# Kernel optimization log

Measured on AMD Instinct MI355X. Metric: run time of the kernel, lower is better.

The kernel has to match this reference:

```python
import jax, jax.numpy as jnp
import numpy as np
from jax import lax

B, T, C = 8, 1025, 512
HEADS = 8
CACHE = 256          # int(dim * cache_ratio)
CLS = 1
L = 256              # gr_cache memory length
H = W = 32           # sqrt(T - CLS)
EPS = 1e-5


def setup_inputs() -> dict:
    key = jax.random.key(0)
    ks = jax.random.split(key, 40)
    def w(k, shape, scale=0.02):
        return jax.random.normal(k, shape, dtype=jnp.float32) * scale
    inp = {}
    inp['x'] = jax.random.normal(ks[0], (B, T, C), dtype=jnp.float32)
    inp['gr_cache'] = jax.random.normal(ks[1], (1, L, CACHE), dtype=jnp.float32)
    # self-attention (dim=512) params, weights stored (in, out)
    inp['Wq1'] = w(ks[2], (C, C)); inp['bq1'] = jnp.zeros((C,), jnp.float32)
    inp['Wk1'] = w(ks[3], (C, C)); inp['bk1'] = jnp.zeros((C,), jnp.float32)
    inp['Wv1'] = w(ks[4], (C, C)); inp['bv1'] = jnp.zeros((C,), jnp.float32)
    inp['Wo1'] = w(ks[5], (C, C)); inp['bo1'] = jnp.zeros((C,), jnp.float32)
    # memory attention (dim=cache_dim=256) params
    inp['Wq2'] = w(ks[6], (CACHE, CACHE)); inp['bq2'] = jnp.zeros((CACHE,), jnp.float32)
    inp['Wk2'] = w(ks[7], (CACHE, CACHE)); inp['bk2'] = jnp.zeros((CACHE,), jnp.float32)
    inp['Wv2'] = w(ks[8], (CACHE, CACHE)); inp['bv2'] = jnp.zeros((CACHE,), jnp.float32)
    inp['Wo2'] = w(ks[9], (CACHE, CACHE)); inp['bo2'] = jnp.zeros((CACHE,), jnp.float32)
    # GRU-style gate linears: in = 2*cache_dim, out = cache_dim
    inp['Wr'] = w(ks[10], (2 * CACHE, CACHE)); inp['br'] = jnp.zeros((CACHE,), jnp.float32)
    inp['Wz'] = w(ks[11], (2 * CACHE, CACHE)); inp['bz'] = jnp.zeros((CACHE,), jnp.float32)
    inp['Wa'] = w(ks[12], (2 * CACHE, CACHE)); inp['ba'] = jnp.zeros((CACHE,), jnp.float32)
    # LayerNorm(cache_dim)
    inp['gamma'] = jnp.ones((CACHE,), jnp.float32)
    inp['beta'] = jnp.zeros((CACHE,), jnp.float32)
    # per-head gate logits, init to -1 as in the module
    inp['lam'] = jnp.full((HEADS,), -1.0, dtype=jnp.float32)
    # grouped conv pos-emb: Conv2d(512, 512, k=3, groups=CACHE) -> (O=512, I/g=2, 3, 3)
    inp['conv_w'] = w(ks[13], (C, C // CACHE, 3, 3))
    inp['conv_b'] = jnp.zeros((C,), jnp.float32)
    return inp


def _mha(q_in, kv_in, Wq, bq, Wk, bk, Wv, bv, Wo, bo):
    Bq, Tq, D = q_in.shape
    Tk = kv_in.shape[1]
    dh = D // HEADS
    q = (q_in @ Wq + bq).reshape(Bq, Tq, HEADS, dh)
    k = (kv_in @ Wk + bk).reshape(Bq, Tk, HEADS, dh)
    v = (kv_in @ Wv + bv).reshape(Bq, Tk, HEADS, dh)
    s = jnp.einsum('bqhd,bkhd->bhqk', q, k) * (1.0 / np.sqrt(dh)).astype(np.float32)
    a = jax.nn.softmax(s, axis=-1)
    o = jnp.einsum('bhqk,bkhd->bqhd', a, v).reshape(Bq, Tq, D)
    return o @ Wo + bo


def reference(x, gr_cache, Wq1, bq1, Wk1, bk1, Wv1, bv1, Wo1, bo1,
              Wq2, bq2, Wk2, bk2, Wv2, bv2, Wo2, bo2,
              Wr, br, Wz, bz, Wa, ba, gamma, beta, lam, conv_w, conv_b):
    B_, T_, C_ = x.shape
    # ---- spatial positional embedding (faithful to torch view->permute quirk) ----
    tok = x[:, CLS:, :].reshape(B_, H, W, C_).transpose(0, 3, 1, 2)   # (B, C, H, W)
    pos = lax.conv_general_dilated(tok, conv_w, (1, 1), 'SAME',
                                   feature_group_count=CACHE,
                                   dimension_numbers=('NCHW', 'OIHW', 'NCHW'))
    pos = pos + conv_b[None, :, None, None]
    pos = pos.reshape(B_, C_, T_ - CLS).transpose(0, 2, 1)            # (B, T-1, C)
    pos = jnp.concatenate([jnp.zeros((B_, CLS, C_), pos.dtype), pos], axis=1)
    # ---- self attention ----
    x_self = _mha(x, x, Wq1, bq1, Wk1, bk1, Wv1, bv1, Wo1, bo1)       # (B, T, C)
    x_self_h = x_self.reshape(B_, T_, HEADS, C_ // HEADS)
    # ---- GRU-style gated cache update ----
    gr = jnp.broadcast_to(gr_cache, (B_, L, CACHE))
    x_summary = x_self[:, :, :CACHE]
    idx = (jnp.arange(L) * T_) // L                                   # nearest interpolate T -> L
    x_summary = x_summary[:, idx, :]                                  # (B, L, CACHE)
    cat = jnp.concatenate([gr, x_summary], axis=-1)
    reset = jax.nn.sigmoid(cat @ Wr + br)
    z = jax.nn.sigmoid(cat @ Wz + bz)
    cat2 = jnp.concatenate([reset * gr, x_summary], axis=-1)
    add = jax.nn.gelu(cat2 @ Wa + ba, approximate=False)
    mu = add.mean(-1, keepdims=True)
    var = ((add - mu) ** 2).mean(-1, keepdims=True)
    add = (add - mu) / jnp.sqrt(var + EPS) * gamma + beta             # LayerNorm
    gr_new = z * add + (1.0 - z) * gr
    # ---- memory attention on first cache_dim channels ----
    x_mem = _mha(x[:, :, :CACHE], gr_new, Wq2, bq2, Wk2, bk2, Wv2, bv2, Wo2, bo2)
    x_mem = x_mem.reshape(B_, T_, HEADS, CACHE // HEADS)
    # ---- per-head alpha blend with zero-padded mem branch ----
    alpha = jax.nn.sigmoid(lam).reshape(1, 1, HEADS, 1)
    pad = jnp.zeros((B_, T_, HEADS, (C_ - CACHE) // HEADS), x.dtype)
    out = (alpha * jnp.concatenate([x_mem, pad], axis=-1)
           + (1.0 - alpha) * x_self_h).reshape(B_, T_, C_) + pos
    return out
```

## Files before the change

kernel.cpp:

```cpp
#include <hip/hip_runtime.h>
#include <math.h>

typedef unsigned short u16;
typedef unsigned int u32;
typedef __attribute__((ext_vector_type(8))) short short8;
typedef __attribute__((ext_vector_type(4))) short short4v;
typedef __attribute__((ext_vector_type(4))) float f32x4;

constexpr int Bc = 8;
constexpr int Tt = 1025;
constexpr int Cc = 512;
constexpr int Hn = 8;
constexpr int CA = 256;
constexpr int Ll = 256;

#if __has_builtin(__builtin_amdgcn_exp2f)
#define EXP2F __builtin_amdgcn_exp2f
#else
#define EXP2F exp2f
#endif

__device__ __forceinline__ u16 f2bf(float f) {
  u32 u = __builtin_bit_cast(u32, f);
  u = (u + 0x7FFFu + ((u >> 16) & 1u)) >> 16;
  return (u16)u;
}
__device__ __forceinline__ u32 pack2f(float lo, float hi) {
  const u32 a = __builtin_bit_cast(u32, hi) + 0x8000u;
  const u32 b = __builtin_bit_cast(u32, lo) + 0x8000u;
  return __builtin_amdgcn_perm(a, b, 0x07060302u);
}

struct WC { const float* s; u16* d; int sN; int sK; int kshift; int tot; };
struct WCP { WC w[11]; };

__global__ void wcast_k(WCP p) {
  const WC a = p.w[blockIdx.y];
  const int kmask = (1 << a.kshift) - 1;
  for (int idx = blockIdx.x * 256 + threadIdx.x; idx < a.tot; idx += gridDim.x * 256) {
    const int k = idx & kmask;
    const int n = idx >> a.kshift;
    a.d[idx] = (k < a.sK) ? f2bf(a.s[(size_t)k * a.sN + n]) : (u16)0;
  }
}

enum { EP_NONE = 0, EP_SIGMOID = 1, EP_GELU = 2 };

struct GemmEpi {
  const float* bias[4];
  int start[4];
  float scale[4];
  int nreg;
};

template <int AF32, int OUTBF, int ACT>
__global__ __launch_bounds__(256) void gemm_mfma(
    const void* __restrict__ Av, int lda,
    const u16* __restrict__ Wt,
    GemmEpi epi,
    void* __restrict__ Cout,
    int M, int N, int K)
{
  __shared__ u16 As[128][32];
  __shared__ u16 Bs[128][32];
  const int tid = threadIdx.x;
  const int m0 = blockIdx.y * 128, n0 = blockIdx.x * 128;
  const int ln = tid & 15, quad = (tid >> 4) & 3, wv = tid >> 6;
  const int wm = (wv & 1) * 64, wn = (wv >> 1) * 64;
  const int sr = tid >> 1;
  const int sk = (tid & 1) * 16;

  f32x4 zf = {0.f, 0.f, 0.f, 0.f};
  f32x4 acc[4][4];
  #pragma unroll
  for (int i = 0; i < 4; i++)
    #pragma unroll
    for (int j = 0; j < 4; j++) acc[i][j] = zf;

  const short8 z8 = {0, 0, 0, 0, 0, 0, 0, 0};

  for (int k0 = 0; k0 < K; k0 += 32) {
    const int gm = m0 + sr;
    short8 a0 = z8, a1 = z8;
    if (gm < M) {
      if (AF32) {
        const float* p = (const float*)Av + (size_t)gm * lda + k0 + sk;
        const float4 f0 = *(const float4*)(p + 0);
        const float4 f1 = *(const float4*)(p + 4);
        const float4 f2 = *(const float4*)(p + 8);
        const float4 f3 = *(const float4*)(p + 12);
        ((u32*)&a0)[0] = pack2f(f0.x, f0.y);
        ((u32*)&a0)[1] = pack2f(f0.z, f0.w);
        ((u32*)&a0)[2] = pack2f(f1.x, f1.y);
        ((u32*)&a0)[3] = pack2f(f1.z, f1.w);
        ((u32*)&a1)[0] = pack2f(f2.x, f2.y);
        ((u32*)&a1)[1] = pack2f(f2.z, f2.w);
        ((u32*)&a1)[2] = pack2f(f3.x, f3.y);
        ((u32*)&a1)[3] = pack2f(f3.z, f3.w);
      } else {
        const u16* p = (const u16*)Av + (size_t)gm * lda + k0 + sk;
        a0 = *(const short8*)p;
        a1 = *(const short8*)(p + 8);
      }
    }
    *(short8*)&As[sr][sk] = a0;
    *(short8*)&As[sr][sk + 8] = a1;
    {
      const u16* q = Wt + (size_t)(n0 + sr) * K + k0 + sk;
      *(short8*)&Bs[sr][sk] = *(const short8*)q;
      *(short8*)&Bs[sr][sk + 8] = *(const short8*)(q + 8);
    }
    __syncthreads();

    short8 af[4], bf[4];
    #pragma unroll
    for (int i = 0; i < 4; i++) af[i] = *(const short8*)&As[wm + i * 16 + ln][quad * 8];
    #pragma unroll
    for (int j = 0; j < 4; j++) bf[j] = *(const short8*)&Bs[wn + j * 16 + ln][quad * 8];
    #pragma unroll
    for (int i = 0; i < 4; i++)
      #pragma unroll
      for (int j = 0; j < 4; j++)
        acc[i][j] = __builtin_amdgcn_mfma_f32_16x16x32_bf16(af[i], bf[j], acc[i][j], 0, 0, 0);
    __syncthreads();
  }

  int ri = 0;
  #pragma unroll
  for (int i = 1; i < 4; i++)
    if (i < epi.nreg && epi.start[i] <= n0) ri = i;
  const float* bp = epi.bias[ri] - epi.start[ri];
  const float sc = epi.scale[ri];

  float bj[4];
  #pragma unroll
  for (int j = 0; j < 4; j++) bj[j] = bp[n0 + wn + j * 16 + ln];

  #pragma unroll
  for (int i = 0; i < 4; i++) {
    #pragma unroll
    for (int r = 0; r < 4; r++) {
      const int gm = m0 + wm + i * 16 + quad * 4 + r;
      if (gm >= M) continue;
      #pragma unroll
      for (int j = 0; j < 4; j++) {
        float v = (acc[i][j][r] + bj[j]) * sc;
        if (ACT == EP_SIGMOID)   v = 1.f / (1.f + __expf(-v));
        else if (ACT == EP_GELU) v = 0.5f * v * (1.f + erff(v * 0.70710678118654752f));
        const size_t off = (size_t)gm * N + n0 + wn + j * 16 + ln;
        if (OUTBF) ((u16*)Cout)[off] = f2bf(v);
        else       ((float*)Cout)[off] = v;
      }
    }
  }
}

template <int DH>
__global__ __launch_bounds__(128) void attn_mfma(
    const u16* __restrict__ Qp, const u16* __restrict__ Kp,
    const u16* __restrict__ Vp, u16* __restrict__ Op,
    int Tq, int Tk, int qbs, int kbs, int obs, int qrs, int krs, int ors)
{
  constexpr int NC = DH / 32;
  constexpr int NM = DH / 16;

  __shared__ u16 Vt[2][DH * 32];
  __shared__ u16 Pb[2 * 32 * 32];

  const int b = blockIdx.y >> 3, h = blockIdx.y & 7;
  const int q0 = blockIdx.x * 64;
  const int tid = threadIdx.x;
  const int wv = tid >> 6;
  const int lane = tid & 63;
  const int ln = lane & 15, quad = lane >> 4;

  const u16* Qb = Qp + (size_t)b * qbs + h * DH;
  const u16* Kb = Kp + (size_t)b * kbs + h * DH;
  const u16* Vb = Vp + (size_t)b * kbs + h * DH;
  u16* Ob = Op + (size_t)b * obs + h * DH;

  const short8 z8 = {0, 0, 0, 0, 0, 0, 0, 0};
  const f32x4 zf = {0.f, 0.f, 0.f, 0.f};

  short8 qf[2][NC];
  #pragma unroll
  for (int qs = 0; qs < 2; qs++) {
    const int gq = q0 + wv * 32 + qs * 16 + ln;
    #pragma unroll
    for (int c = 0; c < NC; c++) {
      if (gq < Tq) qf[qs][c] = *(const short8*)(Qb + (size_t)gq * qrs + c * 32 + quad * 8);
      else         qf[qs][c] = z8;
    }
  }

  f32x4 oacc[2][NM];
  float lsum[2] = {0.f, 0.f};
  #pragma unroll
  for (int qs = 0; qs < 2; qs++)
    #pragma unroll
    for (int c = 0; c < NM; c++) oacc[qs][c] = zf;

  const int vd0 = (tid & 15) * (DH / 16);
  const int vk = (tid >> 4) * 4;
  const int gb = vk >> 3, off = vk & 7;

  const int nfull = Tk >> 5;
  const int nit = (Tk + 31) >> 5;

  for (int it = 0; it < nit; it++) {
    const int k0 = it << 5;
    const bool full = (it < nfull);
    u16* vt = &Vt[it & 1][0];

    short8 kf[2][NC];
    if (full) {
      #pragma unroll
      for (int kc = 0; kc < 2; kc++)
        #pragma unroll
        for (int c = 0; c < NC; c++)
          kf[kc][c] = *(const short8*)(Kb + (size_t)(k0 + kc * 16 + ln) * krs
                                          + c * 32 + quad * 8);
    } else {
      #pragma unroll
      for (int kc = 0; kc < 2; kc++)
        #pragma unroll
        for (int c = 0; c < NC; c++) {
          const int row = k0 + kc * 16 + ln;
          kf[kc][c] = (row < Tk)
              ? *(const short8*)(Kb + (size_t)row * krs + c * 32 + quad * 8)
              : z8;
        }
    }

    {
      short4v vrow[4];
      #pragma unroll
      for (int i2 = 0; i2 < 4; i2++) {
        const int gk = k0 + vk + i2;
        short4v t = {0, 0, 0, 0};
        if (DH == 64) {
          if (full || gk < Tk) t = *(const short4v*)(Vb + (size_t)gk * krs + vd0);
        } else {
          if (full || gk < Tk) {
            ushort2 u = *(const ushort2*)(Vb + (size_t)gk * krs + vd0);
            t[0] = (short)u.x; t[1] = (short)u.y;
          }
        }
        vrow[i2] = t;
      }
      #pragma unroll
      for (int i = 0; i < DH / 16; i++) {
        const int d = vd0 + i;
        const int h2 = (d ^ (d >> 3)) & 3;
        short4v w = {vrow[0][i], vrow[1][i], vrow[2][i], vrow[3][i]};
        *(short4v*)&vt[d * 32 + ((gb ^ h2) << 3) + off] = w;
      }
    }
    __syncthreads();

    #pragma unroll
    for (int qs = 0; qs < 2; qs++) {
      #pragma unroll
      for (int kc = 0; kc < 2; kc++) {
        f32x4 s = zf;
        #pragma unroll
        for (int c = 0; c < NC; c++)
          s = __builtin_amdgcn_mfma_f32_16x16x32_bf16(kf[kc][c], qf[qs][c], s, 0, 0, 0);
        float p0, p1, p2, p3;
        if (full) {
          p0 = EXP2F(s[0]); p1 = EXP2F(s[1]); p2 = EXP2F(s[2]); p3 = EXP2F(s[3]);
        } else {
          const int kb = k0 + kc * 16 + quad * 4;
          p0 = (kb + 0 < Tk) ? EXP2F(s[0]) : 0.f;
          p1 = (kb + 1 < Tk) ? EXP2F(s[1]) : 0.f;
          p2 = (kb + 2 < Tk) ? EXP2F(s[2]) : 0.f;
          p3 = (kb + 3 < Tk) ? EXP2F(s[3]) : 0.f;
        }
        lsum[qs] += (p0 + p1) + (p2 + p3);
        short4v pw;
        ((u32*)&pw)[0] = pack2f(p0, p1);
        ((u32*)&pw)[1] = pack2f(p2, p3);
        const int q = qs * 16 + ln;
        const int g = ((kc * 2 + (quad >> 1)) ^ (ln & 3)) & 3;
        *(short4v*)&Pb[wv * 1024 + q * 32 + (g << 3) + (quad & 1) * 4] = pw;
      }
    }

    short8 pf2[2];
    #pragma unroll
    for (int qs = 0; qs < 2; qs++) {
      const int q = qs * 16 + ln;
      const int g = quad ^ (ln & 3);
      pf2[qs] = *(const short8*)&Pb[wv * 1024 + q * 32 + g * 8];
    }
    #pragma unroll
    for (int c = 0; c < NM; c++) {
      const int d = c * 16 + ln;
      const int g = quad ^ ((d ^ (d >> 3)) & 3);
      const short8 vf = *(const short8*)&vt[d * 32 + g * 8];
      #pragma unroll
      for (int qs = 0; qs < 2; qs++)
        oacc[qs][c] = __builtin_amdgcn_mfma_f32_16x16x32_bf16(pf2[qs], vf, oacc[qs][c], 0, 0, 0);
    }
  }

  float lq[2];
  #pragma unroll
  for (int qs = 0; qs < 2; qs++) {
    float t = lsum[qs];
    t += __shfl_xor(t, 16);
    t += __shfl_xor(t, 32);
    lq[qs] = t;
  }
  #pragma unroll
  for (int qs = 0; qs < 2; qs++) {
    #pragma unroll
    for (int r = 0; r < 4; r++) {
      const float linv = 1.f / __shfl(lq[qs], quad * 4 + r);
      const int gq = q0 + wv * 32 + qs * 16 + quad * 4 + r;
      if (gq >= Tq) continue;
      #pragma unroll
      for (int c = 0; c < NM; c++)
        Ob[(size_t)gq * ors + c * 16 + ln] = f2bf(oacc[qs][c][r] * linv);
    }
  }
}

__global__ __launch_bounds__(256) void conv_combine(
    const float* __restrict__ x, const float* __restrict__ cw,
    const float* __restrict__ cb, const float* __restrict__ x_self,
    const float* __restrict__ x_mem, const float* __restrict__ lam,
    float* __restrict__ out)
{
  const int bh = blockIdx.x;
  const int b = bh >> 5, hh = bh & 31;
  const int c = (blockIdx.y << 8) + threadIdx.x;
  const int ci = c & ~1;
  const int dd = c & 63;
  const int h8 = c >> 6;
  const float alpha = 1.f / (1.f + __expf(-lam[h8]));
  const float bias = cb[c];

  float wgt[2][9];
  #pragma unroll
  for (int ch = 0; ch < 2; ch++)
    #pragma unroll
    for (int k = 0; k < 9; k++) wgt[ch][k] = cw[c * 18 + ch * 9 + k];

  const float* xrow[3];
  bool rv[3];
  #pragma unroll
  for (int r = 0; r < 3; r++) {
    const int h2 = hh + r - 1;
    rv[r] = (unsigned)h2 < 32u;
    xrow[r] = x + ((size_t)(b * Tt) + 1 + h2 * 32) * Cc + ci;
  }

  float2 win[3][3];
  #pragma unroll
  for (int r = 0; r < 3; r++) {
    win[r][0] = make_float2(0.f, 0.f);
    win[r][1] = rv[r] ? *(const float2*)(xrow[r]) : make_float2(0.f, 0.f);
  }

  const size_t bT = (size_t)b * Tt;
  for (int w = 0; w < 32; w++) {
    #pragma unroll
    for (int r = 0; r < 3; r++)
      win[r][2] = (rv[r] && w + 1 < 32) ? *(const float2*)(xrow[r] + (w + 1) * Cc)
                                        : make_float2(0.f, 0.f);
    float pos = bias;
    #pragma unroll
    for (int r = 0; r < 3; r++)
      #pragma unroll
      for (int col = 0; col < 3; col++) {
        pos += win[r][col].x * wgt[0][r * 3 + col];
        pos += win[r][col].y * wgt[1][r * 3 + col];
      }
    const size_t bt = bT + 1 + hh * 32 + w;
    const float mem = (dd < 32) ? x_mem[bt * 256 + h8 * 32 + dd] : 0.f;
    out[bt * 512 + c] = pos + alpha * mem + (1.f - alpha) * x_self[bt * 512 + c];
    #pragma unroll
    for (int r = 0; r < 3; r++) { win[r][0] = win[r][1]; win[r][1] = win[r][2]; }
  }

  if (hh == 0) {
    const float mem = (dd < 32) ? x_mem[bT * 256 + h8 * 32 + dd] : 0.f;
    out[bT * 512 + c] = alpha * mem + (1.f - alpha) * x_self[bT * 512 + c];
  }
}

__global__ void build_cat(const float* __restrict__ gr_cache,
                          const float* __restrict__ x_self,
                          u16* __restrict__ cat)
{
  const int idx = blockIdx.x * 256 + threadIdx.x;
  if (idx >= Bc * Ll * 512) return;
  const int k = idx & 511;
  const int bi = idx >> 9;
  const int i = bi & 255;
  const int b = bi >> 8;
  float v;
  if (k < 256) v = gr_cache[i * 256 + k];
  else         v = x_self[((size_t)(b * Tt + 4 * i)) * Cc + (k - 256)];
  cat[idx] = f2bf(v);
}

__global__ void build_cat2(const float* __restrict__ gr_cache,
                           const float* __restrict__ rzg,
                           u16* __restrict__ cat)
{
  const int idx = blockIdx.x * 256 + threadIdx.x;
  if (idx >= Bc * Ll * 256) return;
  const int k = idx & 255;
  const int bi = idx >> 8;
  const int i = bi & 255;
  cat[(size_t)bi * 512 + k] = f2bf(gr_cache[i * 256 + k] * rzg[(size_t)bi * 512 + k]);
}

__device__ inline float block_sum256(float v, float* red)
{
  #pragma unroll
  for (int o = 32; o >= 1; o >>= 1) v += __shfl_down(v, o);
  const int wid = threadIdx.x >> 6;
  if ((threadIdx.x & 63) == 0) red[wid] = v;
  __syncthreads();
  const float t = red[0] + red[1] + red[2] + red[3];
  __syncthreads();
  return t;
}

__global__ __launch_bounds__(256) void ln_gate(
    const float* __restrict__ add_raw, const float* __restrict__ rzg,
    const float* __restrict__ gr_cache, const float* __restrict__ gamma,
    const float* __restrict__ beta, u16* __restrict__ gr_new)
{
  __shared__ float red[4];
  const int bi = blockIdx.x;
  const int i = bi & 255;
  const int c = threadIdx.x;
  const float v = add_raw[(size_t)bi * 256 + c];
  const float mu = block_sum256(v, red) * (1.f / 256.f);
  const float dv = v - mu;
  const float var = block_sum256(dv * dv, red) * (1.f / 256.f);
  const float nrm = dv * rsqrtf(var + 1e-5f) * gamma[c] + beta[c];
  const float zz = rzg[(size_t)bi * 512 + 256 + c];
  gr_new[(size_t)bi * 256 + c] = f2bf(zz * nrm + (1.f - zz) * gr_cache[i * 256 + c]);
}

extern "C" void kernel_launch(void* const* d_in, const int* in_sizes, int n_in,
                              void* d_out, int out_size, void* d_ws, size_t ws_size,
                              hipStream_t stream)
{
  const float* x        = (const float*)d_in[0];
  const float* gr_cache = (const float*)d_in[1];
  const float* Wq1 = (const float*)d_in[2];  const float* bq1 = (const float*)d_in[3];
  const float* Wk1 = (const float*)d_in[4];  const float* bk1 = (const float*)d_in[5];
  const float* Wv1 = (const float*)d_in[6];  const float* bv1 = (const float*)d_in[7];
  const float* Wo1 = (const float*)d_in[8];  const float* bo1 = (const float*)d_in[9];
  const float* Wq2 = (const float*)d_in[10]; const float* bq2 = (const float*)d_in[11];
  const float* Wk2 = (const float*)d_in[12]; const float* bk2 = (const float*)d_in[13];
  const float* Wv2 = (const float*)d_in[14]; const float* bv2 = (const float*)d_in[15];
  const float* Wo2 = (const float*)d_in[16]; const float* bo2 = (const float*)d_in[17];
  const float* Wr  = (const float*)d_in[18]; const float* br  = (const float*)d_in[19];
  const float* Wz  = (const float*)d_in[20]; const float* bz  = (const float*)d_in[21];
  const float* Wa  = (const float*)d_in[22]; const float* ba  = (const float*)d_in[23];
  const float* gamma = (const float*)d_in[24];
  const float* beta  = (const float*)d_in[25];
  const float* lam   = (const float*)d_in[26];
  const float* conv_w = (const float*)d_in[27];
  const float* conv_b = (const float*)d_in[28];
  float* out = (float*)d_out;

  const int M1 = Bc * Tt;
  const int M2 = Bc * Ll;
  const size_t BTC = (size_t)Bc * Tt * Cc;
  const size_t BLA = (size_t)Bc * Ll * CA;
  const size_t BL2 = (size_t)Bc * Ll * 512;

  char* W = (char*)d_ws;
  u16*   qkvq  = (u16*)(W + 0);
  u16*   att1  = (u16*)(W + 29388800);
  u16*   att2  = (u16*)(W + 29388800);
  float* x_self= (float*)(W + 37785600);
  u16*   cat   = (u16*)(W + 54579200);
  float* rzg   = (float*)(W + 56676352);
  float* addr_ = (float*)(W + 60870656);
  float* x_mem = (float*)(W + 54579200);
  u16*   gr_new= (u16*)(W + 62976000);
  u16*   k2v2  = (u16*)(W + 64024576);
  u16*   wtb   = (u16*)(W + 66121728);

  u16* megaW = wtb;
  u16* o1W   = wtb + 917504;
  u16* rzW   = wtb + 1179648;
  u16* aW    = wtb + 1441792;
  u16* kvW   = wtb + 1572864;
  u16* o2W   = wtb + 1703936;

  const dim3 blk(256);

  {
    WCP p;
    p.w[0]  = {Wq1, megaW + 0,           512, 512, 9, 512 * 512};
    p.w[1]  = {Wk1, megaW + 512 * 512,   512, 512, 9, 512 * 512};
    p.w[2]  = {Wv1, megaW + 1024 * 512,  512, 512, 9, 512 * 512};
    p.w[3]  = {Wq2, megaW + 1536 * 512,  256, 256, 9, 256 * 512};
    p.w[4]  = {Wo1, o1W,                 512, 512, 9, 512 * 512};
    p.w[5]  = {Wr,  rzW + 0,             256, 512, 9, 256 * 512};
    p.w[6]  = {Wz,  rzW + 256 * 512,     256, 512, 9, 256 * 512};
    p.w[7]  = {Wa,  aW,                  256, 512, 9, 256 * 512};
    p.w[8]  = {Wk2, kvW + 0,             256, 256, 8, 256 * 256};
    p.w[9]  = {Wv2, kvW + 256 * 256,     256, 256, 8, 256 * 256};
    p.w[10] = {Wo2, o2W,                 256, 256, 8, 256 * 256};
    wcast_k<<<dim3(64, 11), blk, 0, stream>>>(p);
  }

  const float sQ1 = 0.18033688011112042f;
  const float sQ2 = 0.25503490664918414f;

  {
    GemmEpi e;
    e.bias[0] = bq1; e.start[0] = 0;    e.scale[0] = sQ1;
    e.bias[1] = bk1; e.start[1] = 512;  e.scale[1] = 1.f;
    e.bias[2] = bv1; e.start[2] = 1024; e.scale[2] = 1.f;
    e.bias[3] = bq2; e.start[3] = 1536; e.scale[3] = sQ2;
    e.nreg = 4;
    gemm_mfma<1, 1, EP_NONE><<<dim3(14, 65), blk, 0, stream>>>(
        x, 512, megaW, e, qkvq, M1, 1792, 512);
  }

  attn_mfma<64><<<dim3(17, 64), dim3(128), 0, stream>>>(
      qkvq, qkvq + 512, qkvq + 1024, att1, Tt, Tt,
      Tt * 1792, Tt * 1792, Tt * 512, 1792, 1792, 512);

  {
    GemmEpi e; e.bias[0] = bo1; e.start[0] = 0; e.scale[0] = 1.f; e.nreg = 1;
    gemm_mfma<0, 0, EP_NONE><<<dim3(4, 65), blk, 0, stream>>>(
        att1, 512, o1W, e, x_self, M1, 512, 512);
  }

  build_cat<<<(int)((BL2 + 255) / 256), blk, 0, stream>>>(gr_cache, x_self, cat);
  {
    GemmEpi e;
    e.bias[0] = br; e.start[0] = 0;   e.scale[0] = 1.f;
    e.bias[1] = bz; e.start[1] = 256; e.scale[1] = 1.f;
    e.nreg = 2;
    gemm_mfma<0, 0, EP_SIGMOID><<<dim3(4, 16), blk, 0, stream>>>(
        cat, 512, rzW, e, rzg, M2, 512, 512);
  }
  build_cat2<<<(int)((BLA + 255) / 256), blk, 0, stream>>>(gr_cache, rzg, cat);
  {
    GemmEpi e; e.bias[0] = ba; e.start[0] = 0; e.scale[0] = 1.f; e.nreg = 1;
    gemm_mfma<0, 0, EP_GELU><<<dim3(2, 16), blk, 0, stream>>>(
        cat, 512, aW, e, addr_, M2, 256, 512);
  }
  ln_gate<<<M2, blk, 0, stream>>>(addr_, rzg, gr_cache, gamma, beta, gr_new);

  {
    GemmEpi e;
    e.bias[0] = bk2; e.start[0] = 0;   e.scale[0] = 1.f;
    e.bias[1] = bv2; e.start[1] = 256; e.scale[1] = 1.f;
    e.nreg = 2;
    gemm_mfma<0, 1, EP_NONE><<<dim3(4, 16), blk, 0, stream>>>(
        gr_new, 256, kvW, e, k2v2, M2, 512, 256);
  }

  attn_mfma<32><<<dim3(17, 64), dim3(128), 0, stream>>>(
      qkvq + 1536, k2v2, k2v2 + 256, att2, Tt, Ll,
      Tt * 1792, Ll * 512, Tt * 256, 1792, 512, 256);

  {
    GemmEpi e; e.bias[0] = bo2; e.start[0] = 0; e.scale[0] = 1.f; e.nreg = 1;
    gemm_mfma<0, 0, EP_NONE><<<dim3(2, 65), blk, 0, stream>>>(
        att2, 256, o2W, e, x_mem, M1, 256, 256);
  }

  conv_combine<<<dim3(Bc * 32, 2), blk, 0, stream>>>(x, conv_w, conv_b, x_self,
                                                     x_mem, lam, out);
}
```

Before: 370.3 us.

## Prefetch next K/V tile into registers to overlap global loads with MFMA

The attention loop is restructured so that K fragments and V rows for iteration it+1 are loaded into a second register set while iteration it computes. The loop is unrolled by two and swaps the A/B register buffers between iterations. Out-of-range rows are now clamped to the last valid row instead of being zero-filled, which relies on the existing exp masking to zero their contribution. The aim is to hide global-load latency behind the QK and PV MFMAs, at the cost of extra registers that may reduce occupancy.

```diff
diff --git a/kernel.cpp b/kernel.cpp
--- a/kernel.cpp
+++ b/kernel.cpp
@@ -206,56 +206,48 @@
 
   const int nfull = Tk >> 5;
   const int nit = (Tk + 31) >> 5;
-
-  for (int it = 0; it < nit; it++) {
-    const int k0 = it << 5;
+  const int tkm1 = Tk - 1;
+
+  auto loadK = [&](int it, short8 (&kf)[2][NC]) {
+    #pragma unroll
+    for (int kc = 0; kc < 2; kc++)
+      #pragma unroll
+      for (int c = 0; c < NC; c++) {
+        int row = (it << 5) + kc * 16 + ln;
+        row = row < tkm1 ? row : tkm1;
+        kf[kc][c] = *(const short8*)(Kb + (size_t)row * krs + c * 32 + quad * 8);
+      }
+  };
+  auto loadV = [&](int it, short4v (&vr)[4]) {
+    #pragma unroll
+    for (int i2 = 0; i2 < 4; i2++) {
+      int gk = (it << 5) + vk + i2;
+      gk = gk < tkm1 ? gk : tkm1;
+      short4v t = {0, 0, 0, 0};
+      if (DH == 64) {
+        t = *(const short4v*)(Vb + (size_t)gk * krs + vd0);
+      } else {
+        ushort2 u = *(const ushort2*)(Vb + (size_t)gk * krs + vd0);
+        t[0] = (short)u.x; t[1] = (short)u.y;
+      }
+      vr[i2] = t;
+    }
+  };
+
+  auto body = [&](int it, short8 (&kfC)[2][NC], short4v (&vrC)[4],
+                  short8 (&kfN)[2][NC], short4v (&vrN)[4]) {
     const bool full = (it < nfull);
     u16* vt = &Vt[it & 1][0];
-
-    short8 kf[2][NC];
-    if (full) {
-      #pragma unroll
-      for (int kc = 0; kc < 2; kc++)
-        #pragma unroll
-        for (int c = 0; c < NC; c++)
-          kf[kc][c] = *(const short8*)(Kb + (size_t)(k0 + kc * 16 + ln) * krs
-                                          + c * 32 + quad * 8);
-    } else {
-      #pragma unroll
-      for (int kc = 0; kc < 2; kc++)
-        #pragma unroll
-        for (int c = 0; c < NC; c++) {
-          const int row = k0 + kc * 16 + ln;
-          kf[kc][c] = (row < Tk)
-              ? *(const short8*)(Kb + (size_t)row * krs + c * 32 + quad * 8)
-              : z8;
-        }
-    }
-
-    {
-      short4v vrow[4];
-      #pragma unroll
-      for (int i2 = 0; i2 < 4; i2++) {
-        const int gk = k0 + vk + i2;
-        short4v t = {0, 0, 0, 0};
-        if (DH == 64) {
-          if (full || gk < Tk) t = *(const short4v*)(Vb + (size_t)gk * krs + vd0);
-        } else {
-          if (full || gk < Tk) {
-            ushort2 u = *(const ushort2*)(Vb + (size_t)gk * krs + vd0);
-            t[0] = (short)u.x; t[1] = (short)u.y;
-          }
-        }
-        vrow[i2] = t;
-      }
-      #pragma unroll
-      for (int i = 0; i < DH / 16; i++) {
-        const int d = vd0 + i;
-        const int h2 = (d ^ (d >> 3)) & 3;
-        short4v w = {vrow[0][i], vrow[1][i], vrow[2][i], vrow[3][i]};
-        *(short4v*)&vt[d * 32 + ((gb ^ h2) << 3) + off] = w;
-      }
-    }
+    const int k0 = it << 5;
+
+    #pragma unroll
+    for (int i = 0; i < DH / 16; i++) {
+      const int d = vd0 + i;
+      const int h2 = (d ^ (d >> 3)) & 3;
+      short4v w = {vrC[0][i], vrC[1][i], vrC[2][i], vrC[3][i]};
+      *(short4v*)&vt[d * 32 + ((gb ^ h2) << 3) + off] = w;
+    }
+    if (it + 1 < nit) { loadK(it + 1, kfN); loadV(it + 1, vrN); }
     __syncthreads();
 
     #pragma unroll
@@ -265,7 +257,7 @@
         f32x4 s = zf;
         #pragma unroll
         for (int c = 0; c < NC; c++)
-          s = __builtin_amdgcn_mfma_f32_16x16x32_bf16(kf[kc][c], qf[qs][c], s, 0, 0, 0);
+          s = __builtin_amdgcn_mfma_f32_16x16x32_bf16(kfC[kc][c], qf[qs][c], s, 0, 0, 0);
         float p0, p1, p2, p3;
         if (full) {
           p0 = EXP2F(s[0]); p1 = EXP2F(s[1]); p2 = EXP2F(s[2]); p3 = EXP2F(s[3]);
@@ -302,7 +294,19 @@
       for (int qs = 0; qs < 2; qs++)
         oacc[qs][c] = __builtin_amdgcn_mfma_f32_16x16x32_bf16(pf2[qs], vf, oacc[qs][c], 0, 0, 0);
     }
-  }
+  };
+
+  short8 kfA[2][NC], kfB[2][NC];
+  short4v vrA[4], vrB[4];
+  loadK(0, kfA);
+  loadV(0, vrA);
+
+  int it = 0;
+  for (; it + 1 < nit; it += 2) {
+    body(it, kfA, vrA, kfB, vrB);
+    body(it + 1, kfB, vrB, kfA, vrA);
+  }
+  if (it < nit) body(it, kfA, vrA, kfB, vrB);
 
   float lq[2];
   #pragma unroll
@@ -474,7 +478,6 @@
 
   const int M1 = Bc * Tt;
   const int M2 = Bc * Ll;
-  const size_t BTC = (size_t)Bc * Tt * Cc;
   const size_t BLA = (size_t)Bc * Ll * CA;
   const size_t BL2 = (size_t)Bc * Ll * 512;
 
```

Result: no change. 363.8 us (-1.8%).
